# Optimization experiments

Hardware: AMD Instinct MI355X
Metric: run time of the kernel (lower is better)

Reference implementation:

```python
import jax, jax.numpy as jnp
import numpy as np
from functools import partial

L, B, D_IN, D_MODEL, D_OUT, D_STATE = 2048, 8, 128, 256, 32, 16
D_INNER, DT_RANK, K_CONV = 2 * D_MODEL, D_MODEL // 16, 4
LOG2PI = float(np.log(2.0 * np.pi))


def setup_inputs() -> dict:
    key = jax.random.key(0)
    ks = jax.random.split(key, 16)
    sc = 0.02
    inp = {
        "s": jax.random.normal(ks[0], (L, B, D_IN), jnp.float32),
        "a": jax.random.normal(ks[1], (L, B, D_OUT), jnp.float32),
        # embedding linear
        "W_emb": jax.random.normal(ks[2], (D_IN, D_MODEL), jnp.float32) * sc,
        "b_emb": jnp.zeros((D_MODEL,), jnp.float32),
        # mamba block params
        "norm_w": jnp.ones((D_MODEL,), jnp.float32),
        "W_in": jax.random.normal(ks[3], (D_MODEL, 2 * D_INNER), jnp.float32) * sc,
        "conv_w": jax.random.normal(ks[4], (D_INNER, 1, K_CONV), jnp.float32) * sc,
        "conv_b": jnp.zeros((D_INNER,), jnp.float32),
        "W_x": jax.random.normal(ks[5], (D_INNER, DT_RANK + 2 * D_STATE), jnp.float32) * sc,
        "W_dt": jax.random.normal(ks[6], (DT_RANK, D_INNER), jnp.float32) * sc,
        "b_dt": jnp.full((D_INNER,), -2.0, jnp.float32),  # softplus(-2) ~ small init dt
        "A_log": jnp.broadcast_to(jnp.log(jnp.arange(1, D_STATE + 1, dtype=jnp.float32)), (D_INNER, D_STATE)).copy(),
        "D": jnp.ones((D_INNER,), jnp.float32),
        "W_out": jax.random.normal(ks[7], (D_INNER, D_MODEL), jnp.float32) * sc,
        # action head + log_std
        "W_head": jax.random.normal(ks[8], (D_MODEL, D_OUT), jnp.float32) * sc,
        "b_head": jnp.zeros((D_OUT,), jnp.float32),
        "log_std": jnp.zeros((D_OUT,), jnp.float32),
    }
    return inp


def _rmsnorm(x, w, eps=1e-5):
    return x * jax.lax.rsqrt(jnp.mean(x * x, axis=-1, keepdims=True) + eps) * w


def _silu(x):
    return x * jax.nn.sigmoid(x)


def _mamba_block(x, norm_w, W_in, conv_w, conv_b, W_x, W_dt, b_dt, A_log, D, W_out):
    # x: (B, L, d_model)
    resid = x
    xn = _rmsnorm(x, norm_w)
    xz = xn @ W_in                                  # (B, L, 2*d_inner)
    xp, z = jnp.split(xz, 2, axis=-1)
    # causal depthwise conv over time
    xc = jax.lax.conv_general_dilated(
        xp.transpose(0, 2, 1), conv_w, window_strides=(1,),
        padding=[(K_CONV - 1, 0)], feature_group_count=D_INNER,
        dimension_numbers=("NCH", "OIH", "NCH"))
    xp = _silu((xc + conv_b[None, :, None]).transpose(0, 2, 1))  # (B, L, d_inner)
    # input-dependent SSM params
    x_dbl = xp @ W_x                                # (B, L, dt_rank + 2*d_state)
    dt, Bm, Cm = jnp.split(x_dbl, [DT_RANK, DT_RANK + D_STATE], axis=-1)
    dt = jax.nn.softplus(dt @ W_dt + b_dt)          # (B, L, d_inner)
    A = -jnp.exp(A_log)                             # (d_inner, d_state)

    def step(h, t):
        dt_t, B_t, C_t, x_t = t                     # (B,d_i) (B,d_s) (B,d_s) (B,d_i)
        dA = jnp.exp(dt_t[..., None] * A)           # (B, d_inner, d_state)
        dBx = (dt_t * x_t)[..., None] * B_t[:, None, :]
        h = dA * h + dBx
        y = jnp.einsum("bds,bs->bd", h, C_t)
        return h, y

    h0 = jnp.zeros((x.shape[0], D_INNER, D_STATE), x.dtype)
    tm = lambda u: jnp.moveaxis(u, 1, 0)            # time-major
    _, ys = jax.lax.scan(step, h0, (tm(dt), tm(Bm), tm(Cm), tm(xp)))
    y = jnp.moveaxis(ys, 0, 1) + xp * D             # (B, L, d_inner)
    y = y * _silu(z)
    return y @ W_out + resid


def reference(s, a, W_emb, b_emb, norm_w, W_in, conv_w, conv_b, W_x, W_dt, b_dt,
              A_log, D, W_out, W_head, b_head, log_std):
    x = s @ W_emb + b_emb                           # (L, B, d_model)
    x = x.transpose(1, 0, 2)                        # (B, L, d_model)
    x = _mamba_block(x, norm_w, W_in, conv_w, conv_b, W_x, W_dt, b_dt, A_log, D, W_out)
    x = x.transpose(1, 0, 2)                        # (L, B, d_model)
    mu = x @ W_head + b_head                        # (L, B, d_out)
    # Normal(mu, exp(log_std)).log_prob(a).sum(-1)
    z = (a - mu) * jnp.exp(-log_std)
    logp = -0.5 * z * z - log_std - 0.5 * LOG2PI
    return logp.sum(axis=-1)                        # (L, B)
```

## Files before the change

kernel.cpp:

```cpp
#include <hip/hip_runtime.h>

typedef unsigned short u16;
typedef short bf16x8 __attribute__((ext_vector_type(8)));
typedef float floatx4 __attribute__((ext_vector_type(4)));

#define LSEQ 2048
#define BB 8
#define NTOK (LSEQ*BB)
#define DMODEL 256
#define DINNER 512
#define NSEG 128
#define SEGLEN 16

__device__ __forceinline__ float siluf(float x){ return x / (1.f + __expf(-x)); }
__device__ __forceinline__ float b2f(u16 x){ return __uint_as_float(((unsigned)x) << 16); }
__device__ __forceinline__ u16 f2b(float f){
  unsigned u = __float_as_uint(f);
  unsigned r = (u + 0x7fffu + ((u >> 16) & 1u)) >> 16;
  return (u16)r;
}

__global__ __launch_bounds__(256) void prep_k(
    const float* __restrict__ s, const float* __restrict__ Wemb,
    const float* __restrict__ Win, const float* __restrict__ Wout,
    const float* __restrict__ Wx, const float* __restrict__ Wdt,
    const float* __restrict__ Wh,
    u16* __restrict__ sb, u16* __restrict__ WTe, u16* __restrict__ WTi,
    u16* __restrict__ WTo, u16* __restrict__ WxT, u16* __restrict__ WdtTp,
    u16* __restrict__ WhT)
{
  int g = blockIdx.x, tid = threadIdx.x;
  if (g < 2048) {
    int i = (g*256 + tid)*4;
    float4 v = *(const float4*)&s[i];
    ushort4 o; o.x=f2b(v.x); o.y=f2b(v.y); o.z=f2b(v.z); o.w=f2b(v.w);
    *(ushort4*)&sb[i] = o;
  } else if (g < 2176) {
    int idx = (g-2048)*256 + tid; int n = idx >> 7, k = idx & 127;
    WTe[idx] = f2b(Wemb[(size_t)k*256 + n]);
  } else if (g < 3200) {
    int idx = (g-2176)*256 + tid; int n = idx >> 8, k = idx & 255;
    WTi[idx] = f2b(Win[(size_t)k*1024 + n]);
  } else if (g < 3712) {
    int idx = (g-3200)*256 + tid; int n = idx >> 9, k = idx & 511;
    WTo[idx] = f2b(Wout[(size_t)k*256 + n]);
  } else if (g < 3808) {
    int idx = (g-3712)*256 + tid; int n = idx >> 9, k = idx & 511;
    WxT[idx] = f2b(Wx[(size_t)k*48 + n]);
  } else if (g < 3872) {
    int idx = (g-3808)*256 + tid; int c = idx >> 5, r = idx & 31;
    WdtTp[idx] = (r < 16) ? f2b(Wdt[(size_t)r*512 + c]) : (u16)0;
  } else {
    int idx = (g-3872)*256 + tid; int j = idx >> 8, k = idx & 255;
    WhT[idx] = f2b(Wh[(size_t)k*32 + j]);
  }
}

template<int K, int OUTB>
__global__ __launch_bounds__(256) void gemm_mfma(
    const u16* __restrict__ Ab, const u16* __restrict__ WT,
    const float* __restrict__ bias, void* __restrict__ Cv, int N)
{
  __shared__ u16 Cs[128*136];
  const int tid = threadIdx.x;
  const int wave = tid >> 6, lane = tid & 63;
  const int quad = lane >> 4, l16 = lane & 15;
  const int bm0 = blockIdx.x*128, bn0 = blockIdx.y*128;
  const int bm = bm0 + (wave & 1)*64;
  const int bn = bn0 + (wave >> 1)*64;
  floatx4 acc[4][4];
  #pragma unroll
  for (int r = 0; r < 4; ++r)
    #pragma unroll
    for (int c = 0; c < 4; ++c) acc[r][c] = (floatx4){0.f,0.f,0.f,0.f};

  const u16* Ap = Ab + (size_t)(bm + l16)*K + quad*8;
  const u16* Bp = WT + (size_t)(bn + l16)*K + quad*8;
  #pragma unroll 2
  for (int k0 = 0; k0 < K; k0 += 32) {
    bf16x8 af[4], bf[4];
    #pragma unroll
    for (int r = 0; r < 4; ++r) af[r] = *(const bf16x8*)(Ap + (size_t)r*16*K + k0);
    #pragma unroll
    for (int c = 0; c < 4; ++c) bf[c] = *(const bf16x8*)(Bp + (size_t)c*16*K + k0);
    #pragma unroll
    for (int r = 0; r < 4; ++r)
      #pragma unroll
      for (int c = 0; c < 4; ++c)
        acc[r][c] = __builtin_amdgcn_mfma_f32_16x16x32_bf16(af[r], bf[c], acc[r][c], 0, 0, 0);
  }

  if (OUTB) {
    #pragma unroll
    for (int c = 0; c < 4; ++c) {
      int nl = (wave >> 1)*64 + c*16 + l16;
      float bv = bias ? bias[bn0 + nl] : 0.f;
      #pragma unroll
      for (int r = 0; r < 4; ++r)
        #pragma unroll
        for (int reg = 0; reg < 4; ++reg) {
          int ml = (wave & 1)*64 + r*16 + quad*4 + reg;
          Cs[ml*136 + nl] = f2b(acc[r][c][reg] + bv);
        }
    }
    __syncthreads();
    #pragma unroll
    for (int p = 0; p < 8; ++p) {
      int row = p*16 + (tid >> 4);
      int col = (tid & 15)*8;
      uint4 v = *(const uint4*)&Cs[row*136 + col];
      *(uint4*)&((u16*)Cv)[(size_t)(bm0+row)*N + bn0 + col] = v;
    }
  } else {
    float* Cf = (float*)Cs;
    #pragma unroll
    for (int half = 0; half < 2; ++half) {
      if ((wave & 1) == half) {
        #pragma unroll
        for (int c = 0; c < 4; ++c) {
          int nl = (wave >> 1)*64 + c*16 + l16;
          float bv = bias ? bias[bn0 + nl] : 0.f;
          #pragma unroll
          for (int r = 0; r < 4; ++r)
            #pragma unroll
            for (int reg = 0; reg < 4; ++reg) {
              int ml = r*16 + quad*4 + reg;
              Cf[ml*132 + nl] = acc[r][c][reg] + bv;
            }
        }
      }
      __syncthreads();
      #pragma unroll
      for (int p = 0; p < 8; ++p) {
        int row = p*8 + (tid >> 5);
        int col = (tid & 31)*4;
        float4 v = *(const float4*)&Cf[row*132 + col];
        *(float4*)&((float*)Cv)[(size_t)(bm0 + half*64 + row)*N + bn0 + col] = v;
      }
      __syncthreads();
    }
  }
}

__global__ __launch_bounds__(256) void rmsnorm_k(const float* __restrict__ X,
    const float* __restrict__ w, u16* __restrict__ XNb)
{
  int n = blockIdx.x*4 + (threadIdx.x >> 6);
  int lane = threadIdx.x & 63;
  const float4 x = *(const float4*)&X[(size_t)n*DMODEL + lane*4];
  float ss = x.x*x.x + x.y*x.y + x.z*x.z + x.w*x.w;
  #pragma unroll
  for (int m = 1; m < 64; m <<= 1) ss += __shfl_xor(ss, m);
  float r = rsqrtf(ss * (1.f/DMODEL) + 1e-5f);
  ushort4 o;
  o.x = f2b(x.x * r * w[lane*4+0]);
  o.y = f2b(x.y * r * w[lane*4+1]);
  o.z = f2b(x.z * r * w[lane*4+2]);
  o.w = f2b(x.w * r * w[lane*4+3]);
  *(ushort4*)&XNb[(size_t)n*DMODEL + lane*4] = o;
}

__global__ __launch_bounds__(256) void conv_silu_k(const u16* __restrict__ XZb,
    const float* __restrict__ cw, const float* __restrict__ cb,
    u16* __restrict__ XPb)
{
  int g = blockIdx.x*256 + threadIdx.x;
  int c4 = (g & 127) << 2;
  int n = g >> 7;
  int l = n >> 3;
  float w[4][4];
  #pragma unroll
  for (int i = 0; i < 4; ++i)
    #pragma unroll
    for (int k = 0; k < 4; ++k) w[i][k] = cw[(c4+i)*4 + k];
  float acc[4];
  #pragma unroll
  for (int i = 0; i < 4; ++i) acc[i] = cb[c4+i];
  #pragma unroll
  for (int k = 0; k < 4; ++k) {
    int lp = l - 3 + k;
    if (lp >= 0) {
      const ushort4 xv = *(const ushort4*)&XZb[(size_t)(n - BB*(3-k))*1024 + c4];
      acc[0] = fmaf(w[0][k], b2f(xv.x), acc[0]);
      acc[1] = fmaf(w[1][k], b2f(xv.y), acc[1]);
      acc[2] = fmaf(w[2][k], b2f(xv.z), acc[2]);
      acc[3] = fmaf(w[3][k], b2f(xv.w), acc[3]);
    }
  }
  ushort4 ob;
  ob.x = f2b(siluf(acc[0])); ob.y = f2b(siluf(acc[1]));
  ob.z = f2b(siluf(acc[2])); ob.w = f2b(siluf(acc[3]));
  *(ushort4*)&XPb[(size_t)n*DINNER + c4] = ob;
}

__global__ __launch_bounds__(128) void xdblBC_k(const u16* __restrict__ XPb,
    const u16* __restrict__ WxT,
    float* __restrict__ BM, float* __restrict__ CM, u16* __restrict__ DTRb)
{
  const int tid = threadIdx.x;
  const int wave = tid >> 6, lane = tid & 63;
  const int quad = lane >> 4, l16 = lane & 15;
  const int tok0 = blockIdx.x*32 + wave*16;

  floatx4 acc[3];
  #pragma unroll
  for (int j = 0; j < 3; ++j) acc[j] = (floatx4){0.f,0.f,0.f,0.f};
  const u16* Ap = XPb + (size_t)(tok0 + l16)*DINNER + quad*8;
  const u16* Bp = WxT + (size_t)l16*DINNER + quad*8;
  #pragma unroll
  for (int k0 = 0; k0 < DINNER; k0 += 32) {
    bf16x8 af = *(const bf16x8*)(Ap + k0);
    #pragma unroll
    for (int j = 0; j < 3; ++j) {
      bf16x8 bf = *(const bf16x8*)(Bp + (size_t)j*16*DINNER + k0);
      acc[j] = __builtin_amdgcn_mfma_f32_16x16x32_bf16(af, bf, acc[j], 0, 0, 0);
    }
  }
  #pragma unroll
  for (int reg = 0; reg < 4; ++reg) {
    size_t t = (size_t)(tok0 + quad*4 + reg);
    BM[t*16 + l16] = acc[1][reg];
    CM[t*16 + l16] = acc[2][reg];
    DTRb[t*32 + l16]      = f2b(acc[0][reg]);
    DTRb[t*32 + 16 + l16] = 0;
  }
}

__global__ __launch_bounds__(256) void dtg_k(const u16* __restrict__ DTRb,
    const u16* __restrict__ WdtTp, const float* __restrict__ bdt,
    u16* __restrict__ DTb)
{
  __shared__ u16 Cs[128*136];
  const int tid = threadIdx.x;
  const int wave = tid >> 6, lane = tid & 63;
  const int quad = lane >> 4, l16 = lane & 15;
  const int bm0 = blockIdx.x*128, bn0 = blockIdx.y*128;
  const int bm = bm0 + (wave & 1)*64;
  const int bn = bn0 + (wave >> 1)*64;
  bf16x8 af[4], bf[4];
  #pragma unroll
  for (int r = 0; r < 4; ++r)
    af[r] = *(const bf16x8*)(DTRb + (size_t)(bm + r*16 + l16)*32 + quad*8);
  #pragma unroll
  for (int c = 0; c < 4; ++c)
    bf[c] = *(const bf16x8*)(WdtTp + (size_t)(bn + c*16 + l16)*32 + quad*8);
  #pragma unroll
  for (int c = 0; c < 4; ++c) {
    int nl = (wave >> 1)*64 + c*16 + l16;
    float bd = bdt[bn0 + nl];
    #pragma unroll
    for (int r = 0; r < 4; ++r) {
      floatx4 d = __builtin_amdgcn_mfma_f32_16x16x32_bf16(af[r], bf[c],
                    (floatx4){0.f,0.f,0.f,0.f}, 0, 0, 0);
      #pragma unroll
      for (int reg = 0; reg < 4; ++reg) {
        int ml = (wave & 1)*64 + r*16 + quad*4 + reg;
        float sum = d[reg] + bd;
        Cs[ml*136 + nl] = f2b((sum > 20.f) ? sum : __logf(1.f + __expf(sum)));
      }
    }
  }
  __syncthreads();
  #pragma unroll
  for (int p = 0; p < 8; ++p) {
    int row = p*16 + (tid >> 4);
    int col = (tid & 15)*8;
    uint4 v = *(const uint4*)&Cs[row*136 + col];
    *(uint4*)&DTb[(size_t)(bm0+row)*DINNER + bn0 + col] = v;
  }
}

__global__ __launch_bounds__(256) void scanA_k(const u16* __restrict__ DTb,
    const u16* __restrict__ XPb, const float* __restrict__ BM,
    const float* __restrict__ Alog, u16* __restrict__ HENDb, float* __restrict__ DTS)
{
  __shared__ __align__(16) float Bs[SEGLEN*16];
  const int tid = threadIdx.x;
  const int seg = blockIdx.x, b = blockIdx.y, half = blockIdx.z;
  const int c = half*256 + tid;
  const int t0 = seg*SEGLEN;
  {
    int t = tid >> 4, s = tid & 15;
    Bs[tid] = BM[((size_t)(t0+t)*BB + b)*16 + s];
  }
  float As[16];
  #pragma unroll
  for (int s = 0; s < 16; ++s) As[s] = -__expf(Alog[c*16+s]);
  bool uni = true;
  #pragma unroll
  for (int s = 1; s < 16; ++s)
    uni = uni && (fabsf(As[s] - As[0]*(float)(s+1)) <= 1e-4f*(float)(s+1));
  float h[16];
  #pragma unroll
  for (int s = 0; s < 16; ++s) h[s] = 0.f;
  float dts = 0.f;
  __syncthreads();
  const size_t base = (size_t)t0*BB + b;
  const u16* dtp = DTb + base*DINNER + c;
  const u16* xpp = XPb + base*DINNER + c;
  float dt = b2f(dtp[0]);
  float xp = b2f(xpp[0]);
  for (int t = 0; t < SEGLEN; ++t) {
    float dtn = 0.f, xpn = 0.f;
    if (t+1 < SEGLEN) {
      dtn = b2f(dtp[(size_t)(t+1)*BB*DINNER]);
      xpn = b2f(xpp[(size_t)(t+1)*BB*DINNER]);
    }
    dts += dt;
    float dtx = dt * xp;
    const float4 b0 = *(const float4*)&Bs[t*16+0];
    const float4 b1 = *(const float4*)&Bs[t*16+4];
    const float4 b2 = *(const float4*)&Bs[t*16+8];
    const float4 b3 = *(const float4*)&Bs[t*16+12];
    const float bv[16] = {b0.x,b0.y,b0.z,b0.w, b1.x,b1.y,b1.z,b1.w,
                          b2.x,b2.y,b2.z,b2.w, b3.x,b3.y,b3.z,b3.w};
    float dA[16];
    if (uni) {
      float p = __expf(dt*As[0]);
      dA[0] = p;
      #pragma unroll
      for (int s = 1; s < 16; ++s) dA[s] = dA[s-1]*p;
    } else {
      #pragma unroll
      for (int s = 0; s < 16; ++s) dA[s] = __expf(dt*As[s]);
    }
    #pragma unroll
    for (int s = 0; s < 16; ++s)
      h[s] = fmaf(dA[s], h[s], dtx*bv[s]);
    dt = dtn; xp = xpn;
  }
  u16* hp = &HENDb[(((size_t)seg*BB + b)*DINNER + c)*16];
  #pragma unroll
  for (int q = 0; q < 2; ++q) {
    ushort8plug:;
    ushort4 v0, v1;
    v0.x = f2b(h[q*8+0]); v0.y = f2b(h[q*8+1]); v0.z = f2b(h[q*8+2]); v0.w = f2b(h[q*8+3]);
    v1.x = f2b(h[q*8+4]); v1.y = f2b(h[q*8+5]); v1.z = f2b(h[q*8+6]); v1.w = f2b(h[q*8+7]);
    *(ushort4*)&hp[q*8]     = v0;
    *(ushort4*)&hp[q*8 + 4] = v1;
  }
  DTS[((size_t)seg*BB + b)*DINNER + c] = dts;
}

__global__ __launch_bounds__(256) void stitch_k(u16* __restrict__ HENDb,
    const float* __restrict__ DTS, const float* __restrict__ Alog)
{
  int g = blockIdx.x*256 + threadIdx.x;
  int b = g >> 13;
  int rem = g & 8191;
  int cidx = rem >> 4;
  float A = -__expf(Alog[rem]);
  float h0 = 0.f;
  for (int k = 0; k < NSEG; ++k) {
    size_t idx = (((size_t)k*BB + b) << 13) + rem;
    float hend = b2f(HENDb[idx]);
    HENDb[idx] = f2b(h0);
    float dts = DTS[((size_t)k*BB + b)*DINNER + cidx];
    h0 = fmaf(__expf(dts*A), h0, hend);
  }
}

__global__ __launch_bounds__(256) void scanC_k(const u16* __restrict__ DTb,
    const u16* __restrict__ XPb, const float* __restrict__ BM, const float* __restrict__ CM,
    const u16* __restrict__ XZb, const float* __restrict__ Alog, const float* __restrict__ Dp,
    const u16* __restrict__ H0b, u16* __restrict__ YGb)
{
  __shared__ __align__(16) float Bs[SEGLEN*16];
  __shared__ __align__(16) float Cs[SEGLEN*16];
  const int tid = threadIdx.x;
  const int seg = blockIdx.x, b = blockIdx.y, half = blockIdx.z;
  const int c = half*256 + tid;
  const int t0 = seg*SEGLEN;
  {
    int t = tid >> 4, s = tid & 15;
    size_t nb = ((size_t)(t0+t)*BB + b)*16 + s;
    Bs[tid] = BM[nb];
    Cs[tid] = CM[nb];
  }
  float As[16];
  #pragma unroll
  for (int s = 0; s < 16; ++s) As[s] = -__expf(Alog[c*16+s]);
  bool uni = true;
  #pragma unroll
  for (int s = 1; s < 16; ++s)
    uni = uni && (fabsf(As[s] - As[0]*(float)(s+1)) <= 1e-4f*(float)(s+1));
  float h[16];
  const u16* hp = &H0b[(((size_t)seg*BB + b)*DINNER + c)*16];
  #pragma unroll
  for (int q = 0; q < 4; ++q) {
    ushort4 hv = *(const ushort4*)&hp[q*4];
    h[q*4+0]=b2f(hv.x); h[q*4+1]=b2f(hv.y); h[q*4+2]=b2f(hv.z); h[q*4+3]=b2f(hv.w);
  }
  const float Dv = Dp[c];
  __syncthreads();
  const size_t base = (size_t)t0*BB + b;
  const u16* dtp = DTb + base*DINNER + c;
  const u16* xpp = XPb + base*DINNER + c;
  const u16* zp  = XZb + base*1024 + DINNER + c;
  u16*       ygp = YGb + base*DINNER + c;
  float dt = b2f(dtp[0]);
  float xp = b2f(xpp[0]);
  float zg = b2f(zp[0]);
  for (int t = 0; t < SEGLEN; ++t) {
    float dtn = 0.f, xpn = 0.f, zgn = 0.f;
    if (t+1 < SEGLEN) {
      dtn = b2f(dtp[(size_t)(t+1)*BB*DINNER]);
      xpn = b2f(xpp[(size_t)(t+1)*BB*DINNER]);
      zgn = b2f(zp[(size_t)(t+1)*BB*1024]);
    }
    float dtx = dt * xp;
    const float4 b0 = *(const float4*)&Bs[t*16+0];
    const float4 b1 = *(const float4*)&Bs[t*16+4];
    const float4 b2 = *(const float4*)&Bs[t*16+8];
    const float4 b3 = *(const float4*)&Bs[t*16+12];
    const float4 c0 = *(const float4*)&Cs[t*16+0];
    const float4 c1 = *(const float4*)&Cs[t*16+4];
    const float4 c2 = *(const float4*)&Cs[t*16+8];
    const float4 c3 = *(const float4*)&Cs[t*16+12];
    const float bv[16] = {b0.x,b0.y,b0.z,b0.w, b1.x,b1.y,b1.z,b1.w,
                          b2.x,b2.y,b2.z,b2.w, b3.x,b3.y,b3.z,b3.w};
    const float cv[16] = {c0.x,c0.y,c0.z,c0.w, c1.x,c1.y,c1.z,c1.w,
                          c2.x,c2.y,c2.z,c2.w, c3.x,c3.y,c3.z,c3.w};
    float dA[16];
    if (uni) {
      float p = __expf(dt*As[0]);
      dA[0] = p;
      #pragma unroll
      for (int s = 1; s < 16; ++s) dA[s] = dA[s-1]*p;
    } else {
      #pragma unroll
      for (int s = 0; s < 16; ++s) dA[s] = __expf(dt*As[s]);
    }
    float y0 = 0.f, y1 = 0.f, y2 = 0.f, y3 = 0.f;
    #pragma unroll
    for (int q = 0; q < 4; ++q) {
      h[q*4+0] = fmaf(dA[q*4+0], h[q*4+0], dtx*bv[q*4+0]);
      h[q*4+1] = fmaf(dA[q*4+1], h[q*4+1], dtx*bv[q*4+1]);
      h[q*4+2] = fmaf(dA[q*4+2], h[q*4+2], dtx*bv[q*4+2]);
      h[q*4+3] = fmaf(dA[q*4+3], h[q*4+3], dtx*bv[q*4+3]);
      y0 = fmaf(h[q*4+0], cv[q*4+0], y0);
      y1 = fmaf(h[q*4+1], cv[q*4+1], y1);
      y2 = fmaf(h[q*4+2], cv[q*4+2], y2);
      y3 = fmaf(h[q*4+3], cv[q*4+3], y3);
    }
    float y = (y0+y1) + (y2+y3);
    ygp[(size_t)t*BB*DINNER] = f2b((y + xp*Dv) * siluf(zg));
    dt = dtn; xp = xpn; zg = zgn;
  }
}

__global__ __launch_bounds__(256) void outhead_k(const u16* __restrict__ YGb,
    const u16* __restrict__ WTo, const float* __restrict__ Xres,
    const u16* __restrict__ WhT, const float* __restrict__ bh,
    const float* __restrict__ lstd, const float* __restrict__ a,
    float* __restrict__ out)
{
  __shared__ u16 Xs[64*264];
  const int tid = threadIdx.x;
  const int wave = tid >> 6, lane = tid & 63;
  const int quad = lane >> 4, l16 = lane & 15;
  const int m0 = blockIdx.x*64;
  const int n0 = wave*64;
  floatx4 acc[4][4];
  #pragma unroll
  for (int r = 0; r < 4; ++r)
    #pragma unroll
    for (int c = 0; c < 4; ++c) acc[r][c] = (floatx4){0.f,0.f,0.f,0.f};
  const u16* Ap = YGb + (size_t)(m0 + l16)*DINNER + quad*8;
  const u16* Bp = WTo + (size_t)(n0 + l16)*DINNER + quad*8;
  #pragma unroll 2
  for (int k0 = 0; k0 < DINNER; k0 += 32) {
    bf16x8 af[4], bf[4];
    #pragma unroll
    for (int r = 0; r < 4; ++r) af[r] = *(const bf16x8*)(Ap + (size_t)r*16*DINNER + k0);
    #pragma unroll
    for (int c = 0; c < 4; ++c) bf[c] = *(const bf16x8*)(Bp + (size_t)c*16*DINNER + k0);
    #pragma unroll
    for (int r = 0; r < 4; ++r)
      #pragma unroll
      for (int c = 0; c < 4; ++c)
        acc[r][c] = __builtin_amdgcn_mfma_f32_16x16x32_bf16(af[r], bf[c], acc[r][c], 0, 0, 0);
  }
  #pragma unroll
  for (int c = 0; c < 4; ++c) {
    int n = n0 + c*16 + l16;
    #pragma unroll
    for (int r = 0; r < 4; ++r) {
      #pragma unroll
      for (int reg = 0; reg < 4; ++reg) {
        int ml = r*16 + quad*4 + reg;
        float t = acc[r][c][reg] + Xres[(size_t)(m0 + ml)*DMODEL + n];
        Xs[ml*264 + n] = f2b(t);
      }
    }
  }
  __syncthreads();
  floatx4 mu[2];
  mu[0] = (floatx4){0.f,0.f,0.f,0.f};
  mu[1] = (floatx4){0.f,0.f,0.f,0.f};
  #pragma unroll
  for (int k0 = 0; k0 < DMODEL; k0 += 32) {
    bf16x8 axf = *(const bf16x8*)&Xs[(wave*16 + l16)*264 + k0 + quad*8];
    #pragma unroll
    for (int nt = 0; nt < 2; ++nt) {
      bf16x8 bwf = *(const bf16x8*)(WhT + (size_t)(nt*16 + l16)*DMODEL + k0 + quad*8);
      mu[nt] = __builtin_amdgcn_mfma_f32_16x16x32_bf16(axf, bwf, mu[nt], 0, 0, 0);
    }
  }
  float ls0 = lstd[l16],      els0 = __expf(-ls0), bh0 = bh[l16];
  float ls1 = lstd[16 + l16], els1 = __expf(-ls1), bh1 = bh[16 + l16];
  #pragma unroll
  for (int reg = 0; reg < 4; ++reg) {
    int tok = m0 + wave*16 + quad*4 + reg;
    float m0v = mu[0][reg] + bh0;
    float m1v = mu[1][reg] + bh1;
    float z0 = (a[(size_t)tok*32 + l16]      - m0v) * els0;
    float z1 = (a[(size_t)tok*32 + 16 + l16] - m1v) * els1;
    float t = (-0.5f*z0*z0 - ls0) + (-0.5f*z1*z1 - ls1) - 2.f*0.91893853320467274f;
    t += __shfl_xor(t, 1);
    t += __shfl_xor(t, 2);
    t += __shfl_xor(t, 4);
    t += __shfl_xor(t, 8);
    if (l16 == 0) out[tok] = t;
  }
}

extern "C" void kernel_launch(void* const* d_in, const int* in_sizes, int n_in,
                              void* d_out, int out_size, void* d_ws, size_t ws_size,
                              hipStream_t stream)
{
  const float* s    = (const float*)d_in[0];
  const float* a    = (const float*)d_in[1];
  const float* Wemb = (const float*)d_in[2];
  const float* bemb = (const float*)d_in[3];
  const float* nw   = (const float*)d_in[4];
  const float* Win  = (const float*)d_in[5];
  const float* cw   = (const float*)d_in[6];
  const float* cb   = (const float*)d_in[7];
  const float* Wx   = (const float*)d_in[8];
  const float* Wdt  = (const float*)d_in[9];
  const float* bdt  = (const float*)d_in[10];
  const float* Alog = (const float*)d_in[11];
  const float* Dp   = (const float*)d_in[12];
  const float* Wout = (const float*)d_in[13];
  const float* Wh   = (const float*)d_in[14];
  const float* bh   = (const float*)d_in[15];
  const float* lstd = (const float*)d_in[16];

  float* X    = (float*)d_ws;
  u16*   XZb  = (u16*)(X + (size_t)NTOK*DMODEL);
  u16*   XPb  = XZb + (size_t)NTOK*1024;
  u16*   DTb  = XPb + (size_t)NTOK*DINNER;
  u16*   YGb  = DTb + (size_t)NTOK*DINNER;
  u16*   sb   = YGb + (size_t)NTOK*DINNER;
  u16*   XNb  = sb  + (size_t)NTOK*128;
  u16*   WTe  = XNb + (size_t)NTOK*DMODEL;
  u16*   WTi  = WTe + 256*128;
  u16*   WTo  = WTi + 1024*256;
  u16*   WxT  = WTo + 256*512;
  u16*   WdtTp= WxT + 48*512;
  u16*   WhT  = WdtTp + 512*32;
  u16*   DTRb = WhT + 32*256;
  u16*   HENDb= DTRb + (size_t)NTOK*32;
  float* BM   = (float*)(HENDb + (size_t)NSEG*BB*DINNER*16);
  float* CM   = BM + (size_t)NTOK*16;
  float* DTS  = CM + (size_t)NTOK*16;
  float* out  = (float*)d_out;

  prep_k          <<<3904,        256, 0, stream>>>(s, Wemb, Win, Wout, Wx, Wdt, Wh,
                                                    sb, WTe, WTi, WTo, WxT, WdtTp, WhT);
  gemm_mfma<128,0><<<dim3(128,2), 256, 0, stream>>>(sb,  WTe, bemb,   X,   DMODEL);
  rmsnorm_k       <<<4096,        256, 0, stream>>>(X, nw, XNb);
  gemm_mfma<256,1><<<dim3(128,8), 256, 0, stream>>>(XNb, WTi, nullptr, XZb, 1024);
  conv_silu_k     <<<8192,        256, 0, stream>>>(XZb, cw, cb, XPb);
  xdblBC_k        <<<512,         128, 0, stream>>>(XPb, WxT, BM, CM, DTRb);
  dtg_k           <<<dim3(128,4), 256, 0, stream>>>(DTRb, WdtTp, bdt, DTb);
  scanA_k         <<<dim3(NSEG,BB,2), 256, 0, stream>>>(DTb, XPb, BM, Alog, HENDb, DTS);
  stitch_k        <<<256,         256, 0, stream>>>(HENDb, DTS, Alog);
  scanC_k         <<<dim3(NSEG,BB,2), 256, 0, stream>>>(DTb, XPb, BM, CM, XZb, Alog, Dp, HENDb, YGb);
  outhead_k       <<<256,         256, 0, stream>>>(YGb, WTo, X, WhT, bh, lstd, a, out);
}
```

Before: 277.4 us.

## Stage GEMM operand tiles through LDS instead of direct global loads

The MFMA GEMM kernel and the out-projection/head kernel now load each K-slice of A and B tiles cooperatively into padded shared memory, then read MFMA fragments from LDS. Previously each wave loaded its fragments directly from global memory, duplicating loads across waves that share rows or columns. The new scheme removes that duplication but adds two barriers per K step and has no double buffering, so global latency is no longer hidden by loop unrolling. A stray label is also removed.

```diff
diff --git a/kernel.cpp b/kernel.cpp
--- a/kernel.cpp
+++ b/kernel.cpp
@@ -61,45 +61,53 @@
     const u16* __restrict__ Ab, const u16* __restrict__ WT,
     const float* __restrict__ bias, void* __restrict__ Cv, int N)
 {
-  __shared__ u16 Cs[128*136];
+  __shared__ u16 SH[128*136];
+  u16* As = SH;
+  u16* Bs = SH + 128*40;
   const int tid = threadIdx.x;
   const int wave = tid >> 6, lane = tid & 63;
   const int quad = lane >> 4, l16 = lane & 15;
   const int bm0 = blockIdx.x*128, bn0 = blockIdx.y*128;
-  const int bm = bm0 + (wave & 1)*64;
-  const int bn = bn0 + (wave >> 1)*64;
+  const int wm = (wave & 1)*64, wn = (wave >> 1)*64;
+  const int srow = tid >> 2, sch = (tid & 3)*8;
   floatx4 acc[4][4];
   #pragma unroll
   for (int r = 0; r < 4; ++r)
     #pragma unroll
     for (int c = 0; c < 4; ++c) acc[r][c] = (floatx4){0.f,0.f,0.f,0.f};
 
-  const u16* Ap = Ab + (size_t)(bm + l16)*K + quad*8;
-  const u16* Bp = WT + (size_t)(bn + l16)*K + quad*8;
-  #pragma unroll 2
   for (int k0 = 0; k0 < K; k0 += 32) {
+    #pragma unroll
+    for (int p = 0; p < 2; ++p) {
+      int row = srow + p*64;
+      *(uint4*)&As[row*40 + sch] = *(const uint4*)&Ab[(size_t)(bm0+row)*K + k0 + sch];
+      *(uint4*)&Bs[row*40 + sch] = *(const uint4*)&WT[(size_t)(bn0+row)*K + k0 + sch];
+    }
+    __syncthreads();
     bf16x8 af[4], bf[4];
     #pragma unroll
-    for (int r = 0; r < 4; ++r) af[r] = *(const bf16x8*)(Ap + (size_t)r*16*K + k0);
-    #pragma unroll
-    for (int c = 0; c < 4; ++c) bf[c] = *(const bf16x8*)(Bp + (size_t)c*16*K + k0);
+    for (int r = 0; r < 4; ++r) af[r] = *(const bf16x8*)&As[(wm + r*16 + l16)*40 + quad*8];
+    #pragma unroll
+    for (int c = 0; c < 4; ++c) bf[c] = *(const bf16x8*)&Bs[(wn + c*16 + l16)*40 + quad*8];
     #pragma unroll
     for (int r = 0; r < 4; ++r)
       #pragma unroll
       for (int c = 0; c < 4; ++c)
         acc[r][c] = __builtin_amdgcn_mfma_f32_16x16x32_bf16(af[r], bf[c], acc[r][c], 0, 0, 0);
+    __syncthreads();
   }
 
   if (OUTB) {
+    u16* Cs = SH;
     #pragma unroll
     for (int c = 0; c < 4; ++c) {
-      int nl = (wave >> 1)*64 + c*16 + l16;
+      int nl = wn + c*16 + l16;
       float bv = bias ? bias[bn0 + nl] : 0.f;
       #pragma unroll
       for (int r = 0; r < 4; ++r)
         #pragma unroll
         for (int reg = 0; reg < 4; ++reg) {
-          int ml = (wave & 1)*64 + r*16 + quad*4 + reg;
+          int ml = wm + r*16 + quad*4 + reg;
           Cs[ml*136 + nl] = f2b(acc[r][c][reg] + bv);
         }
     }
@@ -112,13 +120,13 @@
       *(uint4*)&((u16*)Cv)[(size_t)(bm0+row)*N + bn0 + col] = v;
     }
   } else {
-    float* Cf = (float*)Cs;
+    float* Cf = (float*)SH;
     #pragma unroll
     for (int half = 0; half < 2; ++half) {
       if ((wave & 1) == half) {
         #pragma unroll
         for (int c = 0; c < 4; ++c) {
-          int nl = (wave >> 1)*64 + c*16 + l16;
+          int nl = wn + c*16 + l16;
           float bv = bias ? bias[bn0 + nl] : 0.f;
           #pragma unroll
           for (int r = 0; r < 4; ++r)
@@ -332,7 +340,6 @@
   u16* hp = &HENDb[(((size_t)seg*BB + b)*DINNER + c)*16];
   #pragma unroll
   for (int q = 0; q < 2; ++q) {
-    ushort8plug:;
     ushort4 v0, v1;
     v0.x = f2b(h[q*8+0]); v0.y = f2b(h[q*8+1]); v0.z = f2b(h[q*8+2]); v0.w = f2b(h[q*8+3]);
     v1.x = f2b(h[q*8+4]); v1.y = f2b(h[q*8+5]); v1.z = f2b(h[q*8+6]); v1.w = f2b(h[q*8+7]);
@@ -456,30 +463,40 @@
     float* __restrict__ out)
 {
   __shared__ u16 Xs[64*264];
+  u16* As = Xs;
+  u16* Bs = Xs + 64*40;
   const int tid = threadIdx.x;
   const int wave = tid >> 6, lane = tid & 63;
   const int quad = lane >> 4, l16 = lane & 15;
   const int m0 = blockIdx.x*64;
   const int n0 = wave*64;
+  const int srow = tid >> 2, sch = (tid & 3)*8;
   floatx4 acc[4][4];
   #pragma unroll
   for (int r = 0; r < 4; ++r)
     #pragma unroll
     for (int c = 0; c < 4; ++c) acc[r][c] = (floatx4){0.f,0.f,0.f,0.f};
-  const u16* Ap = YGb + (size_t)(m0 + l16)*DINNER + quad*8;
-  const u16* Bp = WTo + (size_t)(n0 + l16)*DINNER + quad*8;
-  #pragma unroll 2
+
   for (int k0 = 0; k0 < DINNER; k0 += 32) {
+    if (srow < 64)
+      *(uint4*)&As[srow*40 + sch] = *(const uint4*)&YGb[(size_t)(m0+srow)*DINNER + k0 + sch];
+    #pragma unroll
+    for (int p = 0; p < 4; ++p) {
+      int row = srow + p*64;
+      *(uint4*)&Bs[row*40 + sch] = *(const uint4*)&WTo[(size_t)row*DINNER + k0 + sch];
+    }
+    __syncthreads();
     bf16x8 af[4], bf[4];
     #pragma unroll
-    for (int r = 0; r < 4; ++r) af[r] = *(const bf16x8*)(Ap + (size_t)r*16*DINNER + k0);
-    #pragma unroll
-    for (int c = 0; c < 4; ++c) bf[c] = *(const bf16x8*)(Bp + (size_t)c*16*DINNER + k0);
+    for (int r = 0; r < 4; ++r) af[r] = *(const bf16x8*)&As[(r*16 + l16)*40 + quad*8];
+    #pragma unroll
+    for (int c = 0; c < 4; ++c) bf[c] = *(const bf16x8*)&Bs[(n0 + c*16 + l16)*40 + quad*8];
     #pragma unroll
     for (int r = 0; r < 4; ++r)
       #pragma unroll
       for (int c = 0; c < 4; ++c)
         acc[r][c] = __builtin_amdgcn_mfma_f32_16x16x32_bf16(af[r], bf[c], acc[r][c], 0, 0, 0);
+    __syncthreads();
   }
   #pragma unroll
   for (int c = 0; c < 4; ++c) {
```

Result: faster. 252.4 us (-9.0%).
